# Optimization experiments

Hardware: AMD Instinct MI355X
Metric: run time of the kernel (lower is better)

Reference implementation:

```python
import jax, jax.numpy as jnp
from jax import lax
import numpy as np

WIN = 7            # skimage structural_similarity default win_size
K1, K2 = 0.01, 0.03
DATA_RANGE = 1.0


def _mean_filter_valid(x, win):
    k = jnp.ones((1, 1, win, win), x.dtype) / (win * win)
    y = lax.conv_general_dilated(x[:, None], k, (1, 1), 'VALID')
    return y[:, 0]


def ssim_loss(img1, img2):
    # img1, img2: (B, H, W); skimage-style SSIM, mean over batch of (1 - ssim)
    f = lambda z: _mean_filter_valid(z, WIN)
    NP = WIN * WIN
    cov_norm = NP / (NP - 1.0)  # unbiased estimator, as in skimage
    ux, uy = f(img1), f(img2)
    uxx, uyy, uxy = f(img1 * img1), f(img2 * img2), f(img1 * img2)
    vx = cov_norm * (uxx - ux * ux)
    vy = cov_norm * (uyy - uy * uy)
    vxy = cov_norm * (uxy - ux * uy)
    C1 = (K1 * DATA_RANGE) ** 2
    C2 = (K2 * DATA_RANGE) ** 2
    S = ((2 * ux * uy + C1) * (2 * vxy + C2)) / ((ux * ux + uy * uy + C1) * (vx + vy + C2))
    return jnp.mean(1.0 - jnp.mean(S, axis=(1, 2)))


def conv2d_same(x, w, b):
    # x: (B, Cin, H, W), w: (Cout, Cin, 3, 3)
    y = lax.conv_general_dilated(x, w, (1, 1), 'SAME')
    return y + b[None, :, None, None]


def maxpool2(x):
    return lax.reduce_window(x, -jnp.inf, lax.max, (1, 1, 2, 2), (1, 1, 2, 2), 'VALID')


def features(x, w1, b1, w2, b2, w3, b3, w4, b4):
    h = jax.nn.relu(conv2d_same(x, w1, b1))
    h = jax.nn.relu(conv2d_same(h, w2, b2))
    h = maxpool2(h)
    h = jax.nn.relu(conv2d_same(h, w3, b3))
    h = jax.nn.relu(conv2d_same(h, w4, b4))
    return h


def _conv_init(key, cout, cin, k=3):
    # torch Conv2d default init: U(-s, s), s = 1/sqrt(cin*k*k)
    kw, kb = jax.random.split(key)
    s = 1.0 / np.sqrt(cin * k * k)
    w = jax.random.uniform(kw, (cout, cin, k, k), jnp.float32, -s, s)
    b = jax.random.uniform(kb, (cout,), jnp.float32, -s, s)
    return w, b


def setup_inputs() -> dict:
    key = jax.random.key(0)
    ks = jax.random.split(key, 6)
    B, H, W = 8, 256, 256
    sr = jax.random.uniform(ks[0], (B, 1, H, W), jnp.float32)
    hr = jax.random.uniform(ks[1], (B, 1, H, W), jnp.float32)
    w1, b1 = _conv_init(ks[2], 64, 1)
    w2, b2 = _conv_init(ks[3], 128, 64)
    w3, b3 = _conv_init(ks[4], 256, 128)
    w4, b4 = _conv_init(ks[5], 256, 256)
    return {"sr": sr, "hr": hr, "w1": w1, "b1": b1, "w2": w2, "b2": b2,
            "w3": w3, "b3": b3, "w4": w4, "b4": b4}


def reference(sr, hr, w1, b1, w2, b2, w3, b3, w4, b4):
    mse_weight, ssim_weight, perceptual_weight = 1.0, 0.5, 0.1
    mse = jnp.mean((sr - hr) ** 2)
    # torch detaches before SSIM (numpy round-trip) -> no gradient through SSIM
    ssim_l = ssim_loss(lax.stop_gradient(sr[:, 0]), lax.stop_gradient(hr[:, 0]))
    sr_f = features(sr, w1, b1, w2, b2, w3, b3, w4, b4)
    hr_f = features(hr, w1, b1, w2, b2, w3, b3, w4, b4)
    perceptual = jnp.mean((sr_f - hr_f) ** 2)
    total = mse_weight * mse + ssim_weight * ssim_l + perceptual_weight * perceptual
    return total, mse, ssim_l, perceptual
```

## Files before the change

### kernel.cpp

```cpp
#include <hip/hip_runtime.h>
#include <hip/hip_bf16.h>

typedef __hip_bfloat16 bf16;
typedef unsigned char u8;
typedef __attribute__((ext_vector_type(4))) float f32x4;
typedef __attribute__((ext_vector_type(8))) int i32x8;
typedef __attribute__((ext_vector_type(4))) unsigned int u32x4;

struct L4 { long a, b, c, d; };
struct U2 { u32x4 x, y; };

typedef __attribute__((address_space(3))) unsigned int lds_uint;
typedef __attribute__((address_space(1))) const unsigned int g_uint;
__device__ inline void gload_lds16(const void* g, void* l) {
    __builtin_amdgcn_global_load_lds((g_uint*)g, (lds_uint*)l, 16, 0, 0);
}

__device__ inline void block_reduce_atomic(float v, float* dst) {
    #pragma unroll
    for (int o = 32; o > 0; o >>= 1) v += __shfl_down(v, o, 64);
    __shared__ float ws[8];
    const int lane = threadIdx.x & 63;
    const int wid  = threadIdx.x >> 6;
    if (lane == 0) ws[wid] = v;
    __syncthreads();
    if (threadIdx.x == 0) {
        float s = 0.f;
        const int nw = (blockDim.x + 63) >> 6;
        for (int i = 0; i < nw; ++i) s += ws[i];
        atomicAdd(dst, s);
    }
}

__global__ void prep_loss_kernel(
    const float* __restrict__ w2, u8* __restrict__ wb2,
    const float* __restrict__ w3, u8* __restrict__ wb3,
    const float* __restrict__ w4, u8* __restrict__ wb4,
    const float* __restrict__ x, const float* __restrict__ y,
    float* __restrict__ accs) {
    const int blk = blockIdx.x;
    if (blk < 3744) {
        const float* w; u8* wb; int CIN, CO, idx;
        if (blk < 288)       { w = w2; wb = wb2; CIN = 64;  CO = 128; idx = blk * 256 + threadIdx.x; }
        else if (blk < 1440) { w = w3; wb = wb3; CIN = 128; CO = 256; idx = (blk - 288) * 256 + threadIdx.x; }
        else                 { w = w4; wb = wb4; CIN = 256; CO = 256; idx = (blk - 1440) * 256 + threadIdx.x; }
        int n = CO * 9 * CIN;
        if (idx >= n) return;
        int t = idx % 9;
        int rest = idx / 9;
        int ci = rest % CIN;
        int co = rest / CIN;
        float v = w[idx];
        int p = ci >> 5, c32 = ci & 31;
        size_t off = (size_t)p * 288 * CO;
        if (t < 8) off += (((size_t)t * 2 + (c32 >> 4)) * CO + co) * 16 + (c32 & 15);
        else       off += 256 * (size_t)CO + (((size_t)(c32 >> 4)) * CO + co) * 16 + (c32 & 15);
        int r = __builtin_amdgcn_cvt_pk_fp8_f32(v, v, 0, false);
        wb[off] = (u8)(r & 0xff);
        return;
    }
    const int lb = blk - 3744;
    float val = 0.f;
    float* dst;
    if (lb < 1960) {
        dst = accs + 1;
        const int b = lb / 245;
        const int t = (lb - b * 245) * 256 + threadIdx.x;
        if (t < 250 * 250) {
            const int i = t / 250, j = t - (t / 250) * 250;
            const float* xp = x + (size_t)b * 65536;
            const float* yp = y + (size_t)b * 65536;
            float sx = 0.f, sy = 0.f, sxx = 0.f, syy = 0.f, sxy = 0.f;
            #pragma unroll
            for (int dy = 0; dy < 7; ++dy) {
                const float* xr = xp + (size_t)(i + dy) * 256 + j;
                const float* yr = yp + (size_t)(i + dy) * 256 + j;
                #pragma unroll
                for (int dx = 0; dx < 7; ++dx) {
                    float a = xr[dx], c = yr[dx];
                    sx += a; sy += c;
                    sxx += a * a; syy += c * c; sxy += a * c;
                }
            }
            const float inv = 1.f / 49.f;
            const float cn  = 49.f / 48.f;
            float ux = sx * inv, uy = sy * inv;
            float vx  = cn * (sxx * inv - ux * ux);
            float vy  = cn * (syy * inv - uy * uy);
            float vxy = cn * (sxy * inv - ux * uy);
            const float C1 = 1e-4f, C2 = 9e-4f;
            val = ((2.f * ux * uy + C1) * (2.f * vxy + C2)) /
                  ((ux * ux + uy * uy + C1) * (vx + vy + C2));
        }
    } else {
        dst = accs + 0;
        int i = (lb - 1960) * 256 + threadIdx.x;
        float4 a = ((const float4*)x)[i];
        float4 b = ((const float4*)y)[i];
        float d0 = a.x - b.x, d1 = a.y - b.y, d2 = a.z - b.z, d3 = a.w - b.w;
        val = d0 * d0 + d1 * d1 + d2 * d2 + d3 * d3;
    }
    block_reduce_atomic(val, dst);
}

__global__ void finalize_kernel(const float* __restrict__ accs, float* __restrict__ out) {
    if (threadIdx.x == 0) {
        float mse    = accs[0] * (1.f / 524288.f);
        float ssim_l = 1.f - accs[1] * (1.f / 500000.f);
        float perc   = accs[2] * (1.f / 33554432.f);
        out[0] = mse + 0.5f * ssim_l + 0.1f * perc;
        out[1] = mse;
        out[2] = ssim_l;
        out[3] = perc;
    }
}

__global__ __launch_bounds__(256) void conv1_kernel(
    const float* __restrict__ sr, const float* __restrict__ hr, int nb, int b0,
    const float* __restrict__ w, const float* __restrict__ bias,
    u8* __restrict__ out) {
    const int H = 256, W = 256;
    const int img = blockIdx.y;
    const float* in = (img < nb) ? (sr + (size_t)(b0 + img) * 65536)
                                 : (hr + (size_t)(b0 + img - nb) * 65536);
    int px = blockIdx.x * 256 + threadIdx.x;
    int y = px >> 8, x = px & 255;
    float p[9];
    #pragma unroll
    for (int dy = 0; dy < 3; ++dy)
        #pragma unroll
        for (int dx = 0; dx < 3; ++dx) {
            int gy = y + dy - 1, gx = x + dx - 1;
            float v = 0.f;
            if ((unsigned)gy < (unsigned)H && (unsigned)gx < (unsigned)W)
                v = in[(size_t)gy * W + gx];
            p[dy * 3 + dx] = v;
        }
    #pragma unroll
    for (int g = 0; g < 8; ++g) {
        float v[8];
        #pragma unroll
        for (int c = 0; c < 8; ++c) {
            int co = g * 8 + c;
            float a = bias[co];
            #pragma unroll
            for (int k = 0; k < 9; ++k) a += w[co * 9 + k] * p[k];
            v[c] = fmaxf(a, 0.f);
        }
        uint2 o;
        int r;
        r = __builtin_amdgcn_cvt_pk_fp8_f32(v[0], v[1], 0, false);
        o.x = __builtin_amdgcn_cvt_pk_fp8_f32(v[2], v[3], r, true);
        r = __builtin_amdgcn_cvt_pk_fp8_f32(v[4], v[5], 0, false);
        o.y = __builtin_amdgcn_cvt_pk_fp8_f32(v[6], v[7], r, true);
        *(uint2*)(out + (((size_t)img * 8 + g) * 65536 + px) * 8) = o;
    }
}

#define BUF_SZ   32768
#define N_ACT_CH 720
#define N_CHUNK  1872
#define WT_BOFF  11520

__global__ __launch_bounds__(256, 2) void conv2_ss(
    const u8* __restrict__ in, const u8* __restrict__ wb,
    const float* __restrict__ bias, u8* __restrict__ out,
    const float* __restrict__ zbuf) {
    const int H = 256, W = 256, CO = 128;
    const size_t HW = 65536;
    const int tid  = threadIdx.x;
    const int lane = tid & 63;
    const int wn   = tid >> 6;
    const int xl = lane & 15;
    const int kq = lane >> 4;
    const int x0 = blockIdx.x * 16;
    const int y0 = blockIdx.y * 16;
    const int img = blockIdx.z >> 1;
    const int co0 = (blockIdx.z & 1) << 6;

    __shared__ __align__(16) char smem[59904];

    f32x4 acc[4][4];
    #pragma unroll
    for (int m = 0; m < 4; ++m)
        #pragma unroll
        for (int n = 0; n < 4; ++n) acc[m][n] = (f32x4){0.f, 0.f, 0.f, 0.f};

    const u8* inp = in + (size_t)img * 8 * HW * 8;

    {
        char* d = smem + tid * 16;
        #pragma unroll
        for (int i = 0; i < 15; ++i) {
            int c = tid + i * 256;
            if (c >= 2 * N_CHUNK) break;
            int ph = (c >= N_CHUNK) ? 1 : 0;
            int c2 = c - ph * N_CHUNK;
            const char* src = (const char*)zbuf;
            if (c2 < N_ACT_CH) {
                int g = c2 / 180, r = c2 - g * 180;
                int row = r / 10, pp = r - row * 10;
                int gy = y0 - 1 + row, colb = x0 - 2 + pp * 2;
                if ((unsigned)gy < (unsigned)H && (unsigned)colb < (unsigned)(W - 1))
                    src = (const char*)(inp + (((size_t)(g + ph * 4)) * HW +
                                              (size_t)gy * W + colb) * 8);
            } else {
                int c3 = c2 - N_ACT_CH;
                size_t o;
                if (c3 < 1024) {
                    int gt = c3 >> 6, co = c3 & 63;
                    o = ((size_t)gt * CO + co0 + co) * 16;
                } else {
                    int c4 = c3 - 1024;
                    int q = c4 >> 6, co = c4 & 63;
                    o = 256 * (size_t)CO + ((size_t)q * CO + co0 + co) * 16;
                }
                src = (const char*)(wb + (size_t)ph * 288 * CO + o);
            }
            gload_lds16(src, d + i * 4096);
        }
    }

    int mxo[2];
    #pragma unroll
    for (int g = 0; g < 2; ++g) {
        int t = g * 4 + kq;
        int dy = t / 3, dx = t - dy * 3;
        mxo[g] = (dy * 20 + dx) * 8;
    }
    const int abase = ((wn * 4) * 20 + xl + 1) * 8;
    const int awmx  = WT_BOFF + kq * 2048 + xl * 16;
    const int aw8   = WT_BOFF + 16384 + (kq >> 1) * 1024 + xl * 16 + (kq & 1) * 8;
    const int ab8   = kq * 2880 + abase + (2 * 20 + 2) * 8;

    __syncthreads();

    #pragma unroll
    for (int p = 0; p < 2; ++p) {
        const char* base = smem + p * 29952;
        #pragma unroll
        for (int g = 0; g < 2; ++g) {
            i32x8 A[4];
            #pragma unroll
            for (int mt = 0; mt < 4; ++mt) {
                const char* pa = base + awmx + g * 8192 + mt * 256;
                U2 u{*(const u32x4*)pa, *(const u32x4*)(pa + 1024)};
                A[mt] = __builtin_bit_cast(i32x8, u);
            }
            #pragma unroll
            for (int nt = 0; nt < 4; ++nt) {
                const char* pb = base + abase + mxo[g] + nt * 160;
                L4 l{*(const long*)pb, *(const long*)(pb + 2880),
                     *(const long*)(pb + 5760), *(const long*)(pb + 8640)};
                i32x8 B = __builtin_bit_cast(i32x8, l);
                #pragma unroll
                for (int mt = 0; mt < 4; ++mt)
                    acc[mt][nt] = __builtin_amdgcn_mfma_scale_f32_16x16x128_f8f6f4(
                        A[mt], B, acc[mt][nt], 0, 0,
                        0, 0x7F7F7F7F, 0, 0x7F7F7F7F);
            }
        }
        {
            long A8[4], B8[4];
            #pragma unroll
            for (int mt = 0; mt < 4; ++mt)
                A8[mt] = *(const long*)(base + aw8 + mt * 256);
            #pragma unroll
            for (int nt = 0; nt < 4; ++nt)
                B8[nt] = *(const long*)(base + ab8 + nt * 160);
            #pragma unroll
            for (int mt = 0; mt < 4; ++mt)
                #pragma unroll
                for (int nt = 0; nt < 4; ++nt)
                    acc[mt][nt] = __builtin_amdgcn_mfma_f32_16x16x32_fp8_fp8(
                        A8[mt], B8[nt], acc[mt][nt], 0, 0, 0);
        }
    }

    const int Hp = H >> 1, Wp = W >> 1;
    const size_t HWp = (size_t)Hp * Wp;
    #pragma unroll
    for (int j = 0; j < 2; ++j) {
        const int py = (y0 + wn * 4 + 2 * j) >> 1;
        const int px = (x0 + xl) >> 1;
        #pragma unroll
        for (int mt = 0; mt < 4; ++mt) {
            const int cb = co0 + mt * 16 + kq * 4;
            const f32x4 bv = *(const f32x4*)(bias + cb);
            float v[4];
            #pragma unroll
            for (int r = 0; r < 4; ++r) {
                float a = acc[mt][2 * j][r] + bv[r];
                float b = acc[mt][2 * j + 1][r] + bv[r];
                float m = fmaxf(a, b);
                m = fmaxf(m, __shfl_xor(m, 1));
                v[r] = fmaxf(m, 0.f);
            }
            if (!(lane & 1)) {
                int w0 = __builtin_amdgcn_cvt_pk_fp8_f32(v[0], v[1], 0, false);
                w0 = __builtin_amdgcn_cvt_pk_fp8_f32(v[2], v[3], w0, true);
                *(int*)(out + (((size_t)img * (CO >> 3) + (cb >> 3)) * HWp +
                               (size_t)py * Wp + px) * 8 + (cb & 7)) = w0;
            }
        }
    }
}

template <int CIN, int EPI>
__global__ __launch_bounds__(256, 2) void conv_mx(
    const u8* __restrict__ in, const u8* __restrict__ wb,
    const float* __restrict__ bias, u8* __restrict__ out,
    int H, int W, int CO,
    const float* __restrict__ zbuf) {
    const int tid  = threadIdx.x;
    const int lane = tid & 63;
    const int wn   = tid >> 6;
    const int xl = lane & 15;
    const int kq = lane >> 4;
    const int x0 = blockIdx.x * 16;
    const int y0 = blockIdx.y * 16;
    const int ngrp = CO >> 6;
    const int img = blockIdx.z / ngrp;
    const int co0 = (blockIdx.z - img * ngrp) << 6;

    __shared__ __align__(16) char smem[2 * BUF_SZ];

    f32x4 acc[4][4];
    #pragma unroll
    for (int m = 0; m < 4; ++m)
        #pragma unroll
        for (int n = 0; n < 4; ++n) acc[m][n] = (f32x4){0.f, 0.f, 0.f, 0.f};

    const size_t HW = (size_t)H * W;
    const u8* inp = in + (size_t)img * (CIN >> 3) * HW * 8;

    const char* srcp[8];
    long adv[8];
    #pragma unroll
    for (int i = 0; i < 8; ++i) {
        int c = tid + i * 256;
        srcp[i] = (const char*)zbuf;
        adv[i] = 0;
        if (c < N_ACT_CH) {
            int g = c / 180, r = c - g * 180;
            int row = r / 10, pp = r - row * 10;
            int gy = y0 - 1 + row, colb = x0 - 2 + pp * 2;
            if ((unsigned)gy < (unsigned)H && (unsigned)colb < (unsigned)(W - 1)) {
                srcp[i] = (const char*)(inp + ((size_t)g * HW + (size_t)gy * W + colb) * 8);
                adv[i] = 4 * HW * 8;
            }
        } else if (c < N_CHUNK) {
            int c2 = c - N_ACT_CH;
            size_t o;
            if (c2 < 1024) {
                int gt = c2 >> 6, co = c2 & 63;
                o = ((size_t)gt * CO + co0 + co) * 16;
            } else {
                int c3 = c2 - 1024;
                int q = c3 >> 6, co = c3 & 63;
                o = 256 * (size_t)CO + ((size_t)q * CO + co0 + co) * 16;
            }
            srcp[i] = (const char*)(wb + o);
            adv[i] = 288 * (size_t)CO;
        }
    }

    int mxo[2];
    #pragma unroll
    for (int g = 0; g < 2; ++g) {
        int t = g * 4 + kq;
        int dy = t / 3, dx = t - dy * 3;
        mxo[g] = (dy * 20 + dx) * 8;
    }
    const int abase = ((wn * 4) * 20 + xl + 1) * 8;
    const int awmx  = WT_BOFF + kq * 2048 + xl * 16;
    const int aw8   = WT_BOFF + 16384 + (kq >> 1) * 1024 + xl * 16 + (kq & 1) * 8;
    const int ab8   = kq * 2880 + abase + (2 * 20 + 2) * 8;

    const int P = CIN / 32;

    {
        char* d = smem + tid * 16;
        #pragma unroll
        for (int i = 0; i < 8; ++i) {
            gload_lds16(srcp[i], d + i * 4096);
            srcp[i] += adv[i];
        }
    }

    for (int p = 0; p < P; ++p) {
        __syncthreads();
        if (p + 1 < P) {
            char* d = smem + ((p + 1) & 1) * BUF_SZ + tid * 16;
            #pragma unroll
            for (int i = 0; i < 8; ++i) {
                gload_lds16(srcp[i], d + i * 4096);
                srcp[i] += adv[i];
            }
        }
        const char* base = smem + (p & 1) * BUF_SZ;
        #pragma unroll
        for (int g = 0; g < 2; ++g) {
            i32x8 A[4];
            #pragma unroll
            for (int mt = 0; mt < 4; ++mt) {
                const char* pa = base + awmx + g * 8192 + mt * 256;
                U2 u{*(const u32x4*)pa, *(const u32x4*)(pa + 1024)};
                A[mt] = __builtin_bit_cast(i32x8, u);
            }
            #pragma unroll
            for (int nt = 0; nt < 4; ++nt) {
                const char* pb = base + abase + mxo[g] + nt * 160;
                L4 l{*(const long*)pb, *(const long*)(pb + 2880),
                     *(const long*)(pb + 5760), *(const long*)(pb + 8640)};
                i32x8 B = __builtin_bit_cast(i32x8, l);
                #pragma unroll
                for (int mt = 0; mt < 4; ++mt)
                    acc[mt][nt] = __builtin_amdgcn_mfma_scale_f32_16x16x128_f8f6f4(
                        A[mt], B, acc[mt][nt], 0, 0,
                        0, 0x7F7F7F7F, 0, 0x7F7F7F7F);
            }
        }
        {
            long A8[4], B8[4];
            #pragma unroll
            for (int mt = 0; mt < 4; ++mt)
                A8[mt] = *(const long*)(base + aw8 + mt * 256);
            #pragma unroll
            for (int nt = 0; nt < 4; ++nt)
                B8[nt] = *(const long*)(base + ab8 + nt * 160);
            #pragma unroll
            for (int mt = 0; mt < 4; ++mt)
                #pragma unroll
                for (int nt = 0; nt < 4; ++nt)
                    acc[mt][nt] = __builtin_amdgcn_mfma_f32_16x16x32_fp8_fp8(
                        A8[mt], B8[nt], acc[mt][nt], 0, 0, 0);
        }
    }

    #pragma unroll
    for (int nt = 0; nt < 4; ++nt) {
        const int y = y0 + wn * 4 + nt;
        #pragma unroll
        for (int mt = 0; mt < 4; ++mt) {
            const int cb = co0 + mt * 16 + kq * 4;
            const f32x4 bv = *(const f32x4*)(bias + cb);
            float v[4];
            #pragma unroll
            for (int r = 0; r < 4; ++r) v[r] = fmaxf(acc[mt][nt][r] + bv[r], 0.f);
            int w0 = __builtin_amdgcn_cvt_pk_fp8_f32(v[0], v[1], 0, false);
            w0 = __builtin_amdgcn_cvt_pk_fp8_f32(v[2], v[3], w0, true);
            *(int*)(out + (((size_t)img * (CO >> 3) + (cb >> 3)) * HW +
                           (size_t)y * W + x0 + xl) * 8 + (cb & 7)) = w0;
        }
    }
}

__global__ __launch_bounds__(256, 2) void conv4_dual(
    const u8* __restrict__ in,
    const u8* __restrict__ wb,
    const float* __restrict__ bias,
    const float* __restrict__ zbuf,
    long hrFix,
    float* __restrict__ pacc) {
    const int H = 128, W = 128, CO = 256;
    const size_t HW = 16384;
    const int tid  = threadIdx.x;
    const int lane = tid & 63;
    const int wn   = tid >> 6;
    const int xl = lane & 15;
    const int kq = lane >> 4;
    const int x0 = blockIdx.x * 16;
    const int y0 = blockIdx.y * 16;
    const int img = blockIdx.z >> 2;
    const int co0 = (blockIdx.z & 3) << 6;

    __shared__ __align__(16) char smem[2 * BUF_SZ];

    f32x4 acc[4][4], sacc[4][4];
    #pragma unroll
    for (int m = 0; m < 4; ++m)
        #pragma unroll
        for (int n = 0; n < 4; ++n) acc[m][n] = (f32x4){0.f, 0.f, 0.f, 0.f};

    const u8* inp = in + (size_t)img * 4194304;

    const char* srcp[8];
    long adv[8];
    #pragma unroll
    for (int i = 0; i < 8; ++i) {
        int c = tid + i * 256;
        srcp[i] = (const char*)zbuf;
        adv[i] = 0;
        if (c < N_ACT_CH) {
            int g = c / 180, r = c - g * 180;
            int row = r / 10, pp = r - row * 10;
            int gy = y0 - 1 + row, colb = x0 - 2 + pp * 2;
            if ((unsigned)gy < (unsigned)H && (unsigned)colb < (unsigned)(W - 1)) {
                srcp[i] = (const char*)(inp + ((size_t)g * HW + (size_t)gy * W + colb) * 8);
                adv[i] = 4 * HW * 8;
            }
        } else if (c < N_CHUNK) {
            int c2 = c - N_ACT_CH;
            size_t o;
            if (c2 < 1024) {
                int gt = c2 >> 6, co = c2 & 63;
                o = ((size_t)gt * CO + co0 + co) * 16;
            } else {
                int c3 = c2 - 1024;
                int q = c3 >> 6, co = c3 & 63;
                o = 256 * (size_t)CO + ((size_t)q * CO + co0 + co) * 16;
            }
            srcp[i] = (const char*)(wb + o);
            adv[i] = 288 * (size_t)CO;
        }
    }

    int mxo[2];
    #pragma unroll
    for (int g = 0; g < 2; ++g) {
        int t = g * 4 + kq;
        int dy = t / 3, dx = t - dy * 3;
        mxo[g] = (dy * 20 + dx) * 8;
    }
    const int abase = ((wn * 4) * 20 + xl + 1) * 8;
    const int awmx  = WT_BOFF + kq * 2048 + xl * 16;
    const int aw8   = WT_BOFF + 16384 + (kq >> 1) * 1024 + xl * 16 + (kq & 1) * 8;
    const int ab8   = kq * 2880 + abase + (2 * 20 + 2) * 8;

    {
        char* d = smem + tid * 16;
        #pragma unroll
        for (int i = 0; i < 8; ++i) {
            gload_lds16(srcp[i], d + i * 4096);
            srcp[i] += adv[i];
        }
    }

    for (int pp = 0; pp < 16; ++pp) {
        __syncthreads();
        if (pp + 1 < 16) {
            if (pp + 1 == 8) {
                #pragma unroll
                for (int i = 0; i < 8; ++i) {
                    if (adv[i] == 524288) srcp[i] += hrFix;
                    else if (adv[i])      srcp[i] -= 8 * 73728;
                }
            }
            char* d = smem + ((pp + 1) & 1) * BUF_SZ + tid * 16;
            #pragma unroll
            for (int i = 0; i < 8; ++i) {
                gload_lds16(srcp[i], d + i * 4096);
                srcp[i] += adv[i];
            }
        }
        const char* base = smem + (pp & 1) * BUF_SZ;
        #pragma unroll
        for (int g = 0; g < 2; ++g) {
            i32x8 A[4];
            #pragma unroll
            for (int mt = 0; mt < 4; ++mt) {
                const char* pa = base + awmx + g * 8192 + mt * 256;
                U2 u{*(const u32x4*)pa, *(const u32x4*)(pa + 1024)};
                A[mt] = __builtin_bit_cast(i32x8, u);
            }
            #pragma unroll
            for (int nt = 0; nt < 4; ++nt) {
                const char* pb = base + abase + mxo[g] + nt * 160;
                L4 l{*(const long*)pb, *(const long*)(pb + 2880),
                     *(const long*)(pb + 5760), *(const long*)(pb + 8640)};
                i32x8 B = __builtin_bit_cast(i32x8, l);
                #pragma unroll
                for (int mt = 0; mt < 4; ++mt)
                    acc[mt][nt] = __builtin_amdgcn_mfma_scale_f32_16x16x128_f8f6f4(
                        A[mt], B, acc[mt][nt], 0, 0,
                        0, 0x7F7F7F7F, 0, 0x7F7F7F7F);
            }
        }
        {
            long A8[4], B8[4];
            #pragma unroll
            for (int mt = 0; mt < 4; ++mt)
                A8[mt] = *(const long*)(base + aw8 + mt * 256);
            #pragma unroll
            for (int nt = 0; nt < 4; ++nt)
                B8[nt] = *(const long*)(base + ab8 + nt * 160);
            #pragma unroll
            for (int mt = 0; mt < 4; ++mt)
                #pragma unroll
                for (int nt = 0; nt < 4; ++nt)
                    acc[mt][nt] = __builtin_amdgcn_mfma_f32_16x16x32_fp8_fp8(
                        A8[mt], B8[nt], acc[mt][nt], 0, 0, 0);
        }
        if (pp == 7) {
            #pragma unroll
            for (int mt = 0; mt < 4; ++mt) {
                const int cb = co0 + mt * 16 + kq * 4;
                const f32x4 bv = *(const f32x4*)(bias + cb);
                #pragma unroll
                for (int nt = 0; nt < 4; ++nt) {
                    #pragma unroll
                    for (int r = 0; r < 4; ++r) {
                        sacc[mt][nt][r] = fmaxf(acc[mt][nt][r] + bv[r], 0.f);
                        acc[mt][nt][r] = 0.f;
                    }
                }
            }
        }
    }

    float s = 0.f;
    #pragma unroll
    for (int mt = 0; mt < 4; ++mt) {
        const int cb = co0 + mt * 16 + kq * 4;
        const f32x4 bv = *(const f32x4*)(bias + cb);
        #pragma unroll
        for (int nt = 0; nt < 4; ++nt) {
            #pragma unroll
            for (int r = 0; r < 4; ++r) {
                float v = fmaxf(acc[mt][nt][r] + bv[r], 0.f);
                float d = sacc[mt][nt][r] - v;
                s += d * d;
            }
        }
    }
    #pragma unroll
    for (int o = 32; o > 0; o >>= 1) s += __shfl_down(s, o, 64);
    __syncthreads();
    if (lane == 0) *(float*)(smem + wn * 4) = s;
    __syncthreads();
    if (tid == 0) {
        float tot = *(float*)(smem) + *(float*)(smem + 4) +
                    *(float*)(smem + 8) + *(float*)(smem + 12);
        atomicAdd(pacc, tot);
    }
}

extern "C" void kernel_launch(void* const* d_in, const int* in_sizes, int n_in,
                              void* d_out, int out_size, void* d_ws, size_t ws_size,
                              hipStream_t stream) {
    const float* sr = (const float*)d_in[0];
    const float* hr = (const float*)d_in[1];
    const float* w1 = (const float*)d_in[2];
    const float* b1 = (const float*)d_in[3];
    const float* w2 = (const float*)d_in[4];
    const float* b2 = (const float*)d_in[5];
    const float* w3 = (const float*)d_in[6];
    const float* b3 = (const float*)d_in[7];
    const float* w4 = (const float*)d_in[8];
    const float* b4 = (const float*)d_in[9];
    float* out = (float*)d_out;

    char* ws = (char*)d_ws;
    size_t off = 0;
    float* accs = (float*)(ws + off); off += 256;
    float* zbuf = (float*)(ws + off); off += 256;
    u8* wb2 = (u8*)(ws + off); off += (size_t)128 * 9 * 64;
    u8* wb3 = (u8*)(ws + off); off += (size_t)256 * 9 * 128;
    u8* wb4 = (u8*)(ws + off); off += (size_t)256 * 9 * 256;
    const size_t fixed = (off + 255) & ~(size_t)255;

    const size_t MB = 1024u * 1024u;
    int nb = 8;
    while (nb > 1 && fixed + (size_t)nb * 12 * MB > ws_size) nb >>= 1;

    u8* A = (u8*)(ws + fixed);
    u8* P = (u8*)(ws + fixed + (size_t)nb * 8 * MB);

    hipMemsetAsync(ws, 0, 512, stream);
    prep_loss_kernel<<<6216, 256, 0, stream>>>(w2, wb2, w3, wb3, w4, wb4, sr, hr, accs);

    for (int b0 = 0; b0 < 8; b0 += nb) {
        const int ni = 2 * nb;
        conv1_kernel<<<dim3(256, ni), 256, 0, stream>>>(sr, hr, nb, b0, w1, b1, A);
        conv2_ss<<<dim3(16, 16, ni * 2), 256, 0, stream>>>(A, wb2, b2, P, zbuf);
        conv_mx<128, 0><<<dim3(8, 8, ni * 4), 256, 0, stream>>>(
            P, wb3, b3, A, 128, 128, 256, zbuf);
        conv4_dual<<<dim3(8, 8, nb * 4), 256, 0, stream>>>(
            A, wb4, b4, zbuf, (long)(nb - 1) * 4194304, accs + 2);
    }

    finalize_kernel<<<1, 1, 0, stream>>>(accs, out);
}
```

Before: 416.3 us.

## Fuse sr/hr passes in conv4 sharing weight tiles, switch activations to 16-channel groups

conv4 previously ran the sr and hr images sequentially over 16 pipeline stages, reloading the weights for each. Now each stage loads the weight slice once and both images' activation tiles, accumulating into two register accumulator sets over 8 stages. The conv3 output layout changes from 8-channel to 16-channel interleaving so B operands come from 16-byte LDS reads instead of four 8-byte reads. This halves weight traffic and barrier count per tile, at the cost of doubled accumulator registers and larger LDS buffers, which may reduce occupancy.

After: 432.8 us. 4.0% more time.

```diff
diff --git a/kernel.cpp b/kernel.cpp
--- a/kernel.cpp
+++ b/kernel.cpp
@@ -450,20 +450,25 @@
             for (int r = 0; r < 4; ++r) v[r] = fmaxf(acc[mt][nt][r] + bv[r], 0.f);
             int w0 = __builtin_amdgcn_cvt_pk_fp8_f32(v[0], v[1], 0, false);
             w0 = __builtin_amdgcn_cvt_pk_fp8_f32(v[2], v[3], w0, true);
-            *(int*)(out + (((size_t)img * (CO >> 3) + (cb >> 3)) * HW +
-                           (size_t)y * W + x0 + xl) * 8 + (cb & 7)) = w0;
-        }
-    }
-}
-
-__global__ __launch_bounds__(256, 2) void conv4_dual(
+            *(int*)(out + (((size_t)img * (CO >> 4) + (cb >> 4)) * HW +
+                           (size_t)y * W + x0 + xl) * 16 + (cb & 15)) = w0;
+        }
+    }
+}
+
+#define C4_ACT  10368
+#define C4_WT   20736
+#define C4_BUF  39168
+#define C4_NCH  2448
+
+__global__ __launch_bounds__(256, 2) void conv4_fused(
     const u8* __restrict__ in,
     const u8* __restrict__ wb,
     const float* __restrict__ bias,
     const float* __restrict__ zbuf,
-    long hrFix,
+    long hrOff,
     float* __restrict__ pacc) {
-    const int H = 128, W = 128, CO = 256;
+    const int W = 128, CO = 256;
     const size_t HW = 16384;
     const int tid  = threadIdx.x;
     const int lane = tid & 63;
@@ -475,86 +480,84 @@
     const int img = blockIdx.z >> 2;
     const int co0 = (blockIdx.z & 3) << 6;
 
-    __shared__ __align__(16) char smem[2 * BUF_SZ];
-
-    f32x4 acc[4][4], sacc[4][4];
+    __shared__ __align__(16) char smem[2 * C4_BUF];
+
+    f32x4 accS[4][4], accH[4][4];
     #pragma unroll
     for (int m = 0; m < 4; ++m)
         #pragma unroll
-        for (int n = 0; n < 4; ++n) acc[m][n] = (f32x4){0.f, 0.f, 0.f, 0.f};
+        for (int n = 0; n < 4; ++n) {
+            accS[m][n] = (f32x4){0.f, 0.f, 0.f, 0.f};
+            accH[m][n] = (f32x4){0.f, 0.f, 0.f, 0.f};
+        }
 
     const u8* inp = in + (size_t)img * 4194304;
 
-    const char* srcp[8];
-    long adv[8];
-    #pragma unroll
-    for (int i = 0; i < 8; ++i) {
+    const char* srcp[10];
+    int adv[10];
+    #pragma unroll
+    for (int i = 0; i < 10; ++i) {
         int c = tid + i * 256;
         srcp[i] = (const char*)zbuf;
         adv[i] = 0;
-        if (c < N_ACT_CH) {
-            int g = c / 180, r = c - g * 180;
-            int row = r / 10, pp = r - row * 10;
-            int gy = y0 - 1 + row, colb = x0 - 2 + pp * 2;
-            if ((unsigned)gy < (unsigned)H && (unsigned)colb < (unsigned)(W - 1)) {
-                srcp[i] = (const char*)(inp + ((size_t)g * HW + (size_t)gy * W + colb) * 8);
-                adv[i] = 4 * HW * 8;
-            }
-        } else if (c < N_CHUNK) {
-            int c2 = c - N_ACT_CH;
+        if (c < 1296) {
+            int c2 = (c >= 648) ? c - 648 : c;
+            int g2 = c2 / 324, rem = c2 - g2 * 324;
+            int row = rem / 18, col = rem - row * 18;
+            int gy = y0 - 1 + row, gx = x0 - 1 + col;
+            if ((unsigned)gy < 128u && (unsigned)gx < 128u) {
+                const u8* ib = inp + ((c >= 648) ? hrOff : 0);
+                srcp[i] = (const char*)(ib + ((size_t)g2 * HW +
+                                              (size_t)gy * W + gx) * 16);
+                adv[i] = 524288;
+            }
+        } else if (c < C4_NCH) {
+            int c3 = c - 1296;
             size_t o;
-            if (c2 < 1024) {
-                int gt = c2 >> 6, co = c2 & 63;
-                o = ((size_t)gt * CO + co0 + co) * 16;
+            if (c3 < 1024) {
+                int kblk = c3 >> 6, co = c3 & 63;
+                o = ((size_t)kblk * CO + co0 + co) * 16;
             } else {
-                int c3 = c2 - 1024;
-                int q = c3 >> 6, co = c3 & 63;
-                o = 256 * (size_t)CO + ((size_t)q * CO + co0 + co) * 16;
+                int c4 = c3 - 1024;
+                int h = c4 >> 6, co = c4 & 63;
+                o = 256 * (size_t)CO + ((size_t)h * CO + co0 + co) * 16;
             }
             srcp[i] = (const char*)(wb + o);
-            adv[i] = 288 * (size_t)CO;
-        }
-    }
-
-    int mxo[2];
+            adv[i] = 73728;
+        }
+    }
+
+    int bmx[2];
     #pragma unroll
     for (int g = 0; g < 2; ++g) {
         int t = g * 4 + kq;
         int dy = t / 3, dx = t - dy * 3;
-        mxo[g] = (dy * 20 + dx) * 8;
-    }
-    const int abase = ((wn * 4) * 20 + xl + 1) * 8;
-    const int awmx  = WT_BOFF + kq * 2048 + xl * 16;
-    const int aw8   = WT_BOFF + 16384 + (kq >> 1) * 1024 + xl * 16 + (kq & 1) * 8;
-    const int ab8   = kq * 2880 + abase + (2 * 20 + 2) * 8;
-
-    {
-        char* d = smem + tid * 16;
-        #pragma unroll
-        for (int i = 0; i < 8; ++i) {
-            gload_lds16(srcp[i], d + i * 4096);
-            srcp[i] += adv[i];
-        }
-    }
-
-    for (int pp = 0; pp < 16; ++pp) {
+        bmx[g] = (dy * 18 + dx) * 16;
+    }
+    const int bnt0 = ((wn * 4) * 18 + xl) * 16;
+    const int awmx = C4_WT + kq * 2048 + xl * 16;
+    const int aw8  = C4_WT + 16384 + (kq >> 1) * 1024 + xl * 16 + (kq & 1) * 8;
+    const int ab8  = ((wn * 4 + 2) * 18 + xl + 2) * 16 +
+                     (kq >> 1) * 5184 + (kq & 1) * 8;
+
+#define C4_STAGE(DB) do {                                            \
+        char* d_ = (DB) + tid * 16;                                  \
+        _Pragma("unroll")                                            \
+        for (int i_ = 0; i_ < 10; ++i_) {                            \
+            if (i_ < 9 || tid < 144) {                               \
+                gload_lds16(srcp[i_], d_ + i_ * 4096);               \
+                srcp[i_] += adv[i_];                                 \
+            }                                                        \
+        } } while (0)
+
+    C4_STAGE(smem);
+
+    for (int pp = 0; pp < 8; ++pp) {
         __syncthreads();
-        if (pp + 1 < 16) {
-            if (pp + 1 == 8) {
-                #pragma unroll
-                for (int i = 0; i < 8; ++i) {
-                    if (adv[i] == 524288) srcp[i] += hrFix;
-                    else if (adv[i])      srcp[i] -= 8 * 73728;
-                }
-            }
-            char* d = smem + ((pp + 1) & 1) * BUF_SZ + tid * 16;
-            #pragma unroll
-            for (int i = 0; i < 8; ++i) {
-                gload_lds16(srcp[i], d + i * 4096);
-                srcp[i] += adv[i];
-            }
-        }
-        const char* base = smem + (pp & 1) * BUF_SZ;
+        if (pp < 7) C4_STAGE(smem + ((pp + 1) & 1) * C4_BUF);
+        const char* base = smem + (pp & 1) * C4_BUF;
+        const char* aS = base;
+        const char* aH = base + C4_ACT;
         #pragma unroll
         for (int g = 0; g < 2; ++g) {
             i32x8 A[4];
@@ -566,48 +569,43 @@
             }
             #pragma unroll
             for (int nt = 0; nt < 4; ++nt) {
-                const char* pb = base + abase + mxo[g] + nt * 160;
-                L4 l{*(const long*)pb, *(const long*)(pb + 2880),
-                     *(const long*)(pb + 5760), *(const long*)(pb + 8640)};
-                i32x8 B = __builtin_bit_cast(i32x8, l);
+                const int bo = bnt0 + nt * 288 + bmx[g];
+                U2 us{*(const u32x4*)(aS + bo), *(const u32x4*)(aS + bo + 5184)};
+                i32x8 BS = __builtin_bit_cast(i32x8, us);
                 #pragma unroll
                 for (int mt = 0; mt < 4; ++mt)
-                    acc[mt][nt] = __builtin_amdgcn_mfma_scale_f32_16x16x128_f8f6f4(
-                        A[mt], B, acc[mt][nt], 0, 0,
+                    accS[mt][nt] = __builtin_amdgcn_mfma_scale_f32_16x16x128_f8f6f4(
+                        A[mt], BS, accS[mt][nt], 0, 0,
                         0, 0x7F7F7F7F, 0, 0x7F7F7F7F);
+                U2 uh{*(const u32x4*)(aH + bo), *(const u32x4*)(aH + bo + 5184)};
+                i32x8 BH = __builtin_bit_cast(i32x8, uh);
+                #pragma unroll
+                for (int mt = 0; mt < 4; ++mt)
+                    accH[mt][nt] = __builtin_amdgcn_mfma_scale_f32_16x16x128_f8f6f4(
+                        A[mt], BH, accH[mt][nt], 0, 0,
+                        0, 0x7F7F7F7F, 0, 0x7F7F7F7F);
             }
         }
         {
-            long A8[4], B8[4];
+            long A8[4];
             #pragma unroll
             for (int mt = 0; mt < 4; ++mt)
                 A8[mt] = *(const long*)(base + aw8 + mt * 256);
             #pragma unroll
-            for (int nt = 0; nt < 4; ++nt)
-                B8[nt] = *(const long*)(base + ab8 + nt * 160);
-            #pragma unroll
-            for (int mt = 0; mt < 4; ++mt)
-                #pragma unroll
-                for (int nt = 0; nt < 4; ++nt)
-                    acc[mt][nt] = __builtin_amdgcn_mfma_f32_16x16x32_fp8_fp8(
-                        A8[mt], B8[nt], acc[mt][nt], 0, 0, 0);
-        }
-        if (pp == 7) {
-            #pragma unroll
-            for (int mt = 0; mt < 4; ++mt) {
-                const int cb = co0 + mt * 16 + kq * 4;
-                const f32x4 bv = *(const f32x4*)(bias + cb);
-                #pragma unroll
-                for (int nt = 0; nt < 4; ++nt) {
-                    #pragma unroll
-                    for (int r = 0; r < 4; ++r) {
-                        sacc[mt][nt][r] = fmaxf(acc[mt][nt][r] + bv[r], 0.f);
-                        acc[mt][nt][r] = 0.f;
-                    }
+            for (int nt = 0; nt < 4; ++nt) {
+                long bs = *(const long*)(aS + ab8 + nt * 288);
+                long bh = *(const long*)(aH + ab8 + nt * 288);
+                #pragma unroll
+                for (int mt = 0; mt < 4; ++mt) {
+                    accS[mt][nt] = __builtin_amdgcn_mfma_f32_16x16x32_fp8_fp8(
+                        A8[mt], bs, accS[mt][nt], 0, 0, 0);
+                    accH[mt][nt] = __builtin_amdgcn_mfma_f32_16x16x32_fp8_fp8(
+                        A8[mt], bh, accH[mt][nt], 0, 0, 0);
                 }
             }
         }
     }
+#undef C4_STAGE
 
     float s = 0.f;
     #pragma unroll
@@ -618,8 +616,9 @@
         for (int nt = 0; nt < 4; ++nt) {
             #pragma unroll
             for (int r = 0; r < 4; ++r) {
-                float v = fmaxf(acc[mt][nt][r] + bv[r], 0.f);
-                float d = sacc[mt][nt][r] - v;
+                float vs = fmaxf(accS[mt][nt][r] + bv[r], 0.f);
+                float vh = fmaxf(accH[mt][nt][r] + bv[r], 0.f);
+                float d = vs - vh;
                 s += d * d;
             }
         }
@@ -676,8 +675,8 @@
         conv2_ss<<<dim3(16, 16, ni * 2), 256, 0, stream>>>(A, wb2, b2, P, zbuf);
         conv_mx<128, 0><<<dim3(8, 8, ni * 4), 256, 0, stream>>>(
             P, wb3, b3, A, 128, 128, 256, zbuf);
-        conv4_dual<<<dim3(8, 8, nb * 4), 256, 0, stream>>>(
-            A, wb4, b4, zbuf, (long)(nb - 1) * 4194304, accs + 2);
+        conv4_fused<<<dim3(8, 8, nb * 4), 256, 0, stream>>>(
+            A, wb4, b4, zbuf, (long)nb * 4194304, accs + 2);
     }
 
     finalize_kernel<<<1, 1, 0, stream>>>(accs, out);
```
